# Kernel tuning notes

Hardware: AMD Instinct MI355X
Metric: run time of the kernel (lower is better)

The kernel has to match this reference:

```python
import jax, jax.numpy as jnp
import numpy as np

WEIGHT = 1.0
EPS = 1e-12  # matches torch F.normalize eps


def setup_inputs() -> dict:
    key = jax.random.key(0)
    k1, k2 = jax.random.split(key)
    B, N, D = 32, 4096, 512
    x = jax.random.normal(k1, (B, N, D), dtype=jnp.float32)
    ref = jax.random.normal(k2, (B, N, D), dtype=jnp.float32)
    return {"x": x, "ref": ref}


def _l2norm(t, axis):
    # torch.nn.functional.normalize: t / max(||t||_2, eps)
    n = jnp.sqrt(jnp.sum(t * t, axis=axis, keepdims=True))
    return t / jnp.maximum(n, EPS)


def reference(x, ref):
    B, N, D = x.shape
    # trace(A @ B^T) == sum(A * B); fused normalize + elementwise + reduce, O(N*D)
    # row-normalized term (dim=1 in torch == last axis per row)
    a_per = jnp.sum(_l2norm(x, 2) * _l2norm(ref, 2), axis=(1, 2)) / N * WEIGHT  # [B]
    # column-normalized term (dim=0 in torch == axis 1 here)
    b_per = jnp.sum(_l2norm(x, 1) * _l2norm(ref, 1), axis=(1, 2)) / D * WEIGHT  # [B]
    a = -jnp.sum(a_per) / B
    b = -jnp.sum(b_per) / B
    return a + b
```

## Files before the change

kernel.cpp:

```cpp
#include <hip/hip_runtime.h>
#include <math.h>


#define BB 32
#define NN 4096
#define DD 512

static constexpr float EPS = 1e-12f;
static constexpr int BPB   = 64;
static constexpr int RPB   = NN / BPB;
static constexpr int NWAVE = 4;
static constexpr int RPW   = RPB / NWAVE;

static constexpr size_t WS_CXX = 0;
static constexpr size_t WS_CRR = (size_t)BB * DD;
static constexpr size_t WS_CXR = (size_t)2 * BB * DD;
static constexpr size_t WS_ROW = (size_t)3 * BB * DD;
static constexpr size_t WS_FLOATS = WS_ROW + 1;

__global__ __launch_bounds__(256) void spl_pass1(
    const float* __restrict__ x, const float* __restrict__ r, float* __restrict__ ws) {
  __shared__ float lds[NWAVE][3][DD];
  __shared__ float ldsrow[NWAVE];

  const int tid  = threadIdx.x;
  const int wave = tid >> 6;
  const int lane = tid & 63;
  const int blk  = blockIdx.x;
  const int b    = blk / BPB;
  const int bib  = blk % BPB;
  const int n0   = bib * RPB + wave * RPW;

  float cxx[8], crr[8], cxr[8];
#pragma unroll
  for (int j = 0; j < 8; ++j) { cxx[j] = 0.f; crr[j] = 0.f; cxr[j] = 0.f; }
  float rowacc = 0.f;

  const size_t base_b = (size_t)b * NN * DD;

  for (int rr = 0; rr < RPW; ++rr) {
    const int n = n0 + rr;
    const float4* xp = (const float4*)(x + base_b + (size_t)n * DD);
    const float4* rp = (const float4*)(r + base_b + (size_t)n * DD);
    float4 x0 = xp[lane];
    float4 x1 = xp[lane + 64];
    float4 r0 = rp[lane];
    float4 r1 = rp[lane + 64];

    float sxx = 0.f, srr = 0.f, sxr = 0.f;
    {
      const float xs[4] = {x0.x, x0.y, x0.z, x0.w};
      const float rs[4] = {r0.x, r0.y, r0.z, r0.w};
#pragma unroll
      for (int j = 0; j < 4; ++j) {
        const float pxx = xs[j] * xs[j];
        const float prr = rs[j] * rs[j];
        const float pxr = xs[j] * rs[j];
        sxx += pxx; srr += prr; sxr += pxr;
        cxx[j] += pxx; crr[j] += prr; cxr[j] += pxr;
      }
    }
    {
      const float xs[4] = {x1.x, x1.y, x1.z, x1.w};
      const float rs[4] = {r1.x, r1.y, r1.z, r1.w};
#pragma unroll
      for (int j = 0; j < 4; ++j) {
        const float pxx = xs[j] * xs[j];
        const float prr = rs[j] * rs[j];
        const float pxr = xs[j] * rs[j];
        sxx += pxx; srr += prr; sxr += pxr;
        cxx[4 + j] += pxx; crr[4 + j] += prr; cxr[4 + j] += pxr;
      }
    }
#pragma unroll
    for (int off = 1; off < 64; off <<= 1) {
      sxx += __shfl_xor(sxx, off, 64);
      srr += __shfl_xor(srr, off, 64);
      sxr += __shfl_xor(sxr, off, 64);
    }
    const float nx = fmaxf(sqrtf(sxx), EPS);
    const float nr = fmaxf(sqrtf(srr), EPS);
    rowacc += sxr / (nx * nr);
  }

#pragma unroll
  for (int k = 0; k < 2; ++k) {
#pragma unroll
    for (int j = 0; j < 4; ++j) {
      const int d = k * 256 + lane * 4 + j;
      lds[wave][0][d] = cxx[k * 4 + j];
      lds[wave][1][d] = crr[k * 4 + j];
      lds[wave][2][d] = cxr[k * 4 + j];
    }
  }
  if (lane == 0) ldsrow[wave] = rowacc;
  __syncthreads();

  float* cxx_g = ws + WS_CXX;
  float* crr_g = ws + WS_CRR;
  float* cxr_g = ws + WS_CXR;
  for (int d = tid; d < DD; d += 256) {
    float s0 = 0.f, s1 = 0.f, s2 = 0.f;
#pragma unroll
    for (int w = 0; w < NWAVE; ++w) {
      s0 += lds[w][0][d];
      s1 += lds[w][1][d];
      s2 += lds[w][2][d];
    }
    atomicAdd(&cxx_g[b * DD + d], s0);
    atomicAdd(&crr_g[b * DD + d], s1);
    atomicAdd(&cxr_g[b * DD + d], s2);
  }
  if (tid == 0) {
    atomicAdd(ws + WS_ROW, ldsrow[0] + ldsrow[1] + ldsrow[2] + ldsrow[3]);
  }
}

__global__ __launch_bounds__(256) void spl_pass2(const float* __restrict__ ws,
                                                 float* __restrict__ out) {
  const int tid = threadIdx.x;
  const float* cxx_g = ws + WS_CXX;
  const float* crr_g = ws + WS_CRR;
  const float* cxr_g = ws + WS_CXR;

  float acc = 0.f;
  for (int i = tid; i < BB * DD; i += 256) {
    const float sxx = cxx_g[i];
    const float srr = crr_g[i];
    const float sxr = cxr_g[i];
    const float nx = fmaxf(sqrtf(sxx), EPS);
    const float nr = fmaxf(sqrtf(srr), EPS);
    acc += sxr / (nx * nr);
  }
#pragma unroll
  for (int off = 1; off < 64; off <<= 1) acc += __shfl_xor(acc, off, 64);

  __shared__ float wsum[4];
  if ((tid & 63) == 0) wsum[tid >> 6] = acc;
  __syncthreads();
  if (tid == 0) {
    const float colsum = wsum[0] + wsum[1] + wsum[2] + wsum[3];
    const float rowsum = ws[WS_ROW];
    const float a = -rowsum / ((float)NN * (float)BB);
    const float b = -colsum / ((float)DD * (float)BB);
    out[0] = a + b;
  }
}

extern "C" void kernel_launch(void* const* d_in, const int* in_sizes, int n_in,
                              void* d_out, int out_size, void* d_ws, size_t ws_size,
                              hipStream_t stream) {
  const float* x = (const float*)d_in[0];
  const float* r = (const float*)d_in[1];
  float* out = (float*)d_out;
  float* ws = (float*)d_ws;

  (void)in_sizes; (void)n_in; (void)out_size; (void)ws_size;

  hipMemsetAsync(ws, 0, WS_FLOATS * sizeof(float), stream);
  spl_pass1<<<BB * BPB, 256, 0, stream>>>(x, r, ws);
  spl_pass2<<<1, 256, 0, stream>>>(ws, out);
}
```

Measured before the change: 145.2 us.

## Batch row reductions through LDS and halve rows per block

Rows per block drop from 64 to 32, doubling the grid to 4096 blocks. Per-row wave-wide shuffle reductions are replaced by a batched scheme: partial sums for 4 rows go to LDS, then 16-lane groups each reduce one row, so one shuffle chain serves four rows. Column partials are staged through a smaller LDS buffer in two halves with float4 stores to cut shared memory use. Each row result is now replicated across 16 lanes, which the final 0.0625 scale corrects. The cost is more global atomics from the doubled block count and extra barriers.

```diff
diff --git a/kernel.cpp b/kernel.cpp
--- a/kernel.cpp
+++ b/kernel.cpp
@@ -7,10 +7,12 @@
 #define DD 512
 
 static constexpr float EPS = 1e-12f;
-static constexpr int BPB   = 64;
-static constexpr int RPB   = NN / BPB;
+static constexpr int ROWS_PER_BLOCK = 32;
+static constexpr int BPB   = NN / ROWS_PER_BLOCK;
 static constexpr int NWAVE = 4;
-static constexpr int RPW   = RPB / NWAVE;
+static constexpr int RPW   = ROWS_PER_BLOCK / NWAVE;
+static constexpr int SUB   = 4;
+static constexpr int NSUB  = RPW / SUB;
 
 static constexpr size_t WS_CXX = 0;
 static constexpr size_t WS_CRR = (size_t)BB * DD;
@@ -20,7 +22,7 @@
 
 __global__ __launch_bounds__(256) void spl_pass1(
     const float* __restrict__ x, const float* __restrict__ r, float* __restrict__ ws) {
-  __shared__ float lds[NWAVE][3][DD];
+  __shared__ float smem[NWAVE * 3 * SUB * 64];
   __shared__ float ldsrow[NWAVE];
 
   const int tid  = threadIdx.x;
@@ -29,7 +31,7 @@
   const int blk  = blockIdx.x;
   const int b    = blk / BPB;
   const int bib  = blk % BPB;
-  const int n0   = bib * RPB + wave * RPW;
+  const int n0   = bib * ROWS_PER_BLOCK + wave * RPW;
 
   float cxx[8], crr[8], cxr[8];
 #pragma unroll
@@ -37,82 +39,107 @@
   float rowacc = 0.f;
 
   const size_t base_b = (size_t)b * NN * DD;
+  const int rgrp = lane >> 4;
+  const int rj   = lane & 15;
 
-  for (int rr = 0; rr < RPW; ++rr) {
-    const int n = n0 + rr;
-    const float4* xp = (const float4*)(x + base_b + (size_t)n * DD);
-    const float4* rp = (const float4*)(r + base_b + (size_t)n * DD);
-    float4 x0 = xp[lane];
-    float4 x1 = xp[lane + 64];
-    float4 r0 = rp[lane];
-    float4 r1 = rp[lane + 64];
+  for (int s = 0; s < NSUB; ++s) {
+#pragma unroll
+    for (int rr = 0; rr < SUB; ++rr) {
+      const int n = n0 + s * SUB + rr;
+      const float4* xp = (const float4*)(x + base_b + (size_t)n * DD);
+      const float4* rp = (const float4*)(r + base_b + (size_t)n * DD);
+      const float4 x0 = xp[lane];
+      const float4 x1 = xp[lane + 64];
+      const float4 r0 = rp[lane];
+      const float4 r1 = rp[lane + 64];
 
-    float sxx = 0.f, srr = 0.f, sxr = 0.f;
-    {
-      const float xs[4] = {x0.x, x0.y, x0.z, x0.w};
-      const float rs[4] = {r0.x, r0.y, r0.z, r0.w};
+      float sxx = 0.f, srr = 0.f, sxr = 0.f;
+      {
+        const float xs[4] = {x0.x, x0.y, x0.z, x0.w};
+        const float rs[4] = {r0.x, r0.y, r0.z, r0.w};
 #pragma unroll
-      for (int j = 0; j < 4; ++j) {
-        const float pxx = xs[j] * xs[j];
-        const float prr = rs[j] * rs[j];
-        const float pxr = xs[j] * rs[j];
-        sxx += pxx; srr += prr; sxr += pxr;
-        cxx[j] += pxx; crr[j] += prr; cxr[j] += pxr;
+        for (int j = 0; j < 4; ++j) {
+          const float pxx = xs[j] * xs[j];
+          const float prr = rs[j] * rs[j];
+          const float pxr = xs[j] * rs[j];
+          sxx += pxx; srr += prr; sxr += pxr;
+          cxx[j] += pxx; crr[j] += prr; cxr[j] += pxr;
+        }
       }
+      {
+        const float xs[4] = {x1.x, x1.y, x1.z, x1.w};
+        const float rs[4] = {r1.x, r1.y, r1.z, r1.w};
+#pragma unroll
+        for (int j = 0; j < 4; ++j) {
+          const float pxx = xs[j] * xs[j];
+          const float prr = rs[j] * rs[j];
+          const float pxr = xs[j] * rs[j];
+          sxx += pxx; srr += prr; sxr += pxr;
+          cxx[4 + j] += pxx; crr[4 + j] += prr; cxr[4 + j] += pxr;
+        }
+      }
+      smem[((wave * 3 + 0) * SUB + rr) * 64 + lane] = sxx;
+      smem[((wave * 3 + 1) * SUB + rr) * 64 + lane] = srr;
+      smem[((wave * 3 + 2) * SUB + rr) * 64 + lane] = sxr;
     }
-    {
-      const float xs[4] = {x1.x, x1.y, x1.z, x1.w};
-      const float rs[4] = {r1.x, r1.y, r1.z, r1.w};
+
+    float vs[3];
 #pragma unroll
-      for (int j = 0; j < 4; ++j) {
-        const float pxx = xs[j] * xs[j];
-        const float prr = rs[j] * rs[j];
-        const float pxr = xs[j] * rs[j];
-        sxx += pxx; srr += prr; sxr += pxr;
-        cxx[4 + j] += pxx; crr[4 + j] += prr; cxr[4 + j] += pxr;
-      }
+    for (int m = 0; m < 3; ++m) {
+      const float* p = &smem[((wave * 3 + m) * SUB + rgrp) * 64];
+      float v = p[rj] + p[rj + 16] + p[rj + 32] + p[rj + 48];
+#pragma unroll
+      for (int off = 1; off < 16; off <<= 1) v += __shfl_xor(v, off, 64);
+      vs[m] = v;
     }
-#pragma unroll
-    for (int off = 1; off < 64; off <<= 1) {
-      sxx += __shfl_xor(sxx, off, 64);
-      srr += __shfl_xor(srr, off, 64);
-      sxr += __shfl_xor(sxr, off, 64);
-    }
-    const float nx = fmaxf(sqrtf(sxx), EPS);
-    const float nr = fmaxf(sqrtf(srr), EPS);
-    rowacc += sxr / (nx * nr);
+    const float nx = fmaxf(sqrtf(vs[0]), EPS);
+    const float nr = fmaxf(sqrtf(vs[1]), EPS);
+    rowacc += vs[2] / (nx * nr);
   }
 
 #pragma unroll
-  for (int k = 0; k < 2; ++k) {
+  for (int off = 1; off < 64; off <<= 1) rowacc += __shfl_xor(rowacc, off, 64);
+  if (lane == 0) ldsrow[wave] = rowacc;
+
+  __syncthreads();
+  {
+    float4* cb = (float4*)smem;
 #pragma unroll
-    for (int j = 0; j < 4; ++j) {
-      const int d = k * 256 + lane * 4 + j;
-      lds[wave][0][d] = cxx[k * 4 + j];
-      lds[wave][1][d] = crr[k * 4 + j];
-      lds[wave][2][d] = cxr[k * 4 + j];
+    for (int m = 0; m < 3; ++m) {
+      const float* c = (m == 0) ? cxx : (m == 1) ? crr : cxr;
+      cb[(wave * 3 + m) * 64 + lane] = make_float4(c[0], c[1], c[2], c[3]);
     }
   }
-  if (lane == 0) ldsrow[wave] = rowacc;
   __syncthreads();
+  for (int i = tid; i < 768; i += 256) {
+    const int m = i >> 8;
+    const int d = i & 255;
+    const float sum = smem[(0 * 3 + m) * 256 + d] + smem[(1 * 3 + m) * 256 + d] +
+                      smem[(2 * 3 + m) * 256 + d] + smem[(3 * 3 + m) * 256 + d];
+    atomicAdd(ws + (size_t)m * BB * DD + (size_t)b * DD + d, sum);
+  }
 
-  float* cxx_g = ws + WS_CXX;
-  float* crr_g = ws + WS_CRR;
-  float* cxr_g = ws + WS_CXR;
-  for (int d = tid; d < DD; d += 256) {
-    float s0 = 0.f, s1 = 0.f, s2 = 0.f;
+  __syncthreads();
+  {
+    float4* cb = (float4*)smem;
 #pragma unroll
-    for (int w = 0; w < NWAVE; ++w) {
-      s0 += lds[w][0][d];
-      s1 += lds[w][1][d];
-      s2 += lds[w][2][d];
+    for (int m = 0; m < 3; ++m) {
+      const float* c = (m == 0) ? cxx : (m == 1) ? crr : cxr;
+      cb[(wave * 3 + m) * 64 + lane] = make_float4(c[4], c[5], c[6], c[7]);
     }
-    atomicAdd(&cxx_g[b * DD + d], s0);
-    atomicAdd(&crr_g[b * DD + d], s1);
-    atomicAdd(&cxr_g[b * DD + d], s2);
   }
+  __syncthreads();
+  for (int i = tid; i < 768; i += 256) {
+    const int m = i >> 8;
+    const int d = i & 255;
+    const float sum = smem[(0 * 3 + m) * 256 + d] + smem[(1 * 3 + m) * 256 + d] +
+                      smem[(2 * 3 + m) * 256 + d] + smem[(3 * 3 + m) * 256 + d];
+    atomicAdd(ws + (size_t)m * BB * DD + (size_t)b * DD + 256 + d, sum);
+  }
+
   if (tid == 0) {
-    atomicAdd(ws + WS_ROW, ldsrow[0] + ldsrow[1] + ldsrow[2] + ldsrow[3]);
+    const float tot = (ldsrow[0] + ldsrow[1] + ldsrow[2] + ldsrow[3]) * 0.0625f;
+    atomicAdd(ws + WS_ROW, tot);
   }
 }
 
```

New measurement: 159.5 us. 9.8% more time.
